# Kernel tuning notes

Hardware: AMD Instinct MI355X
Metric: run time of the kernel (lower is better)

Reference implementation:

```python
import jax, jax.numpy as jnp
import numpy as np

NUM_GRAPHS = 512
NODES_PER_GRAPH = 30
IN_CH = 8
HID = 64
NUM_LAYERS = 5
BRANCHES = 41
BN_EPS = 1e-5


def setup_inputs() -> dict:
    key = jax.random.key(0)
    ks = jax.random.split(key, 16)
    N = NUM_GRAPHS * NODES_PER_GRAPH
    x = jax.random.normal(ks[0], (N, IN_CH), jnp.float32)
    branch_u = jax.random.randint(ks[1], (BRANCHES,), 0, NODES_PER_GRAPH, jnp.int32)
    branch_v = jax.random.randint(ks[2], (BRANCHES,), 0, NODES_PER_GRAPH, jnp.int32)
    # Build bidirectional edge_index from the per-graph branch list + graph offsets
    offsets = (jnp.arange(NUM_GRAPHS, dtype=jnp.int32) * NODES_PER_GRAPH)
    u = (branch_u[None, :] + offsets[:, None]).reshape(-1)
    v = (branch_v[None, :] + offsets[:, None]).reshape(-1)
    edge_index = jnp.stack([jnp.concatenate([u, v]), jnp.concatenate([v, u])], axis=0)  # [2, E]
    s = 0.05
    inp = {
        'x': x, 'edge_index': edge_index, 'branch_u': branch_u, 'branch_v': branch_v,
        'num_graphs': NUM_GRAPHS,
        'Wp': jax.random.normal(ks[3], (IN_CH, HID), jnp.float32) * s,
        'bp': jnp.zeros((HID,), jnp.float32),
        'W1': jax.random.normal(ks[4], (NUM_LAYERS, 2 * HID, 32), jnp.float32) * s,
        'b1': jnp.zeros((NUM_LAYERS, 32), jnp.float32),
        'W2': jax.random.normal(ks[5], (NUM_LAYERS, 32, HID * HID), jnp.float32) * s,
        'b2': jnp.zeros((NUM_LAYERS, HID * HID), jnp.float32),
        'Wr': jax.random.normal(ks[6], (NUM_LAYERS, HID, HID), jnp.float32) * s,
        'br': jnp.zeros((NUM_LAYERS, HID), jnp.float32),
        'gamma': jnp.ones((NUM_LAYERS, HID), jnp.float32),
        'beta': jnp.zeros((NUM_LAYERS, HID), jnp.float32),
        'rmean': jax.random.normal(ks[7], (NUM_LAYERS, HID), jnp.float32) * s,
        'rvar': jax.random.uniform(ks[8], (NUM_LAYERS, HID), jnp.float32) + 0.5,
        'Wm1': jax.random.normal(ks[9], (2 * HID, HID), jnp.float32) * s,
        'bm1': jnp.zeros((HID,), jnp.float32),
        'Wm2': jax.random.normal(ks[10], (HID, 1), jnp.float32) * s,
        'bm2': jnp.zeros((1,), jnp.float32),
    }
    return inp


def reference(x, edge_index, branch_u, branch_v, num_graphs,
              Wp, bp, W1, b1, W2, b2, Wr, br,
              gamma, beta, rmean, rvar, Wm1, bm1, Wm2, bm2):
    N = x.shape[0]
    src, dst = edge_index[0], edge_index[1]  # messages flow src -> dst
    h = x @ Wp + bp  # [N, H]
    # in-degree for mean aggregation (clamped to avoid div-by-zero on isolated nodes)
    deg = jax.ops.segment_sum(jnp.ones(src.shape, h.dtype), dst, num_segments=N)
    deg = jnp.maximum(deg, 1.0)[:, None]
    for l in range(NUM_LAYERS):
        res = h
        ea = jnp.concatenate([h[src], h[dst]], axis=-1)              # [E, 2H] edge_attr
        w = jax.nn.relu(ea @ W1[l] + b1[l]) @ W2[l] + b2[l]          # [E, H*H]
        w = w.reshape(-1, HID, HID)                                  # [E, in, out]
        msg = jnp.einsum('eh,eho->eo', h[src], w)                    # gather + bmm
        agg = jax.ops.segment_sum(msg, dst, num_segments=N) / deg    # scatter-mean
        h2 = agg + h @ Wr[l] + br[l]                                 # NNConv root weight + bias
        # BatchNorm1d (eval mode: running stats)
        h2 = (h2 - rmean[l]) * (gamma[l] / jnp.sqrt(rvar[l] + BN_EPS)) + beta[l]
        h = jax.nn.relu(h2) + res                                    # dropout off (eval) + residual
    offsets = jnp.arange(num_graphs, dtype=src.dtype) * NODES_PER_GRAPH
    u_idx = (branch_u[None, :] + offsets[:, None]).reshape(-1)
    v_idx = (branch_v[None, :] + offsets[:, None]).reshape(-1)
    ef = jnp.concatenate([h[u_idx], h[v_idx]], axis=-1)              # [G*41, 2H]
    out = jax.nn.relu(ef @ Wm1 + bm1) @ Wm2 + bm2                    # [G*41, 1]
    return out
```

## Files before the change

kernel.cpp:

```cpp
#include <hip/hip_runtime.h>


typedef float f32x4 __attribute__((ext_vector_type(4)));
typedef _Float16 f16x8 __attribute__((ext_vector_type(8)));
typedef _Float16 f16x4 __attribute__((ext_vector_type(4)));

#define MFMA16(a, b, c) __builtin_amdgcn_mfma_f32_16x16x32_f16((a), (b), (c), 0, 0, 0)

#define WS_W2S 0u
#define WS_W1S 1351680u
#define WS_WRS 1392640u
#define WS_BNS 1433600u
#define WS_BNH 1434880u
#define WS_WM1H 1436160u
#define WS_WM1L 1452544u

__device__ inline f16x8 ld_frag_g(const _Float16* p) {
  union { uint4 u; f16x8 f; } c;
  c.u = *(const uint4*)p;
  return c.f;
}
__device__ inline f16x8 ld_frag_s(const _Float16* p) { return *(const f16x8*)p; }

__global__ __launch_bounds__(256) void prep_kernel(
    const float* __restrict__ W1, const float* __restrict__ W2,
    const float* __restrict__ b2, const float* __restrict__ Wr,
    const float* __restrict__ gamma, const float* __restrict__ beta,
    const float* __restrict__ rmean, const float* __restrict__ rvar,
    const float* __restrict__ Wm1, unsigned char* __restrict__ ws) {
  __shared__ __align__(16) float tile[32][68];
  const int tid = threadIdx.x;
  if (blockIdx.x < 330) {
    int l = blockIdx.x / 66, jb = blockIdx.x % 66;
    int s = tid >> 3, n0 = (tid & 7) * 8;
    int j = jb * 32 + s;
    const float* srcp = (j < 2048)
        ? (W2 + (size_t)l * 131072 + (size_t)j * 64 + n0)
        : (b2 + (size_t)l * 4096 + (size_t)(j - 2048) * 64 + n0);
    *(f32x4*)&tile[s][n0] = *(const f32x4*)srcp;
    *(f32x4*)&tile[s][n0 + 4] = *(const f32x4*)(srcp + 4);
    __syncthreads();
    int n = tid >> 2, sb = (tid & 3) * 8;
    f16x8 hv;
#pragma unroll
    for (int u = 0; u < 8; ++u) hv[u] = (_Float16)tile[sb + u][n];
    _Float16* dst = (_Float16*)(ws + WS_W2S) +
                    (size_t)l * 135168 + (size_t)jb * 2048 + n * 32 + sb;
    *(f16x8*)dst = hv;
    return;
  }
  int idx = (blockIdx.x - 330) * 256 + tid;
  _Float16* W1s = (_Float16*)(ws + WS_W1S);
  _Float16* Wrs = (_Float16*)(ws + WS_WRS);
  float* bns = (float*)(ws + WS_BNS);
  float* bnh = (float*)(ws + WS_BNH);
  _Float16* Wm1h = (_Float16*)(ws + WS_WM1H);
  _Float16* Wm1l = (_Float16*)(ws + WS_WM1L);
  if (idx < 20480) {
    int l = idx / 4096, r = idx % 4096;
    int t = r >> 10, n = (r >> 5) & 31, s2 = r & 31;
    int j = t * 32 + s2;
    W1s[idx] = (_Float16)W1[l * 4096 + j * 32 + n];
  } else if (idx < 40960) {
    int i3 = idx - 20480;
    int l = i3 / 4096, r = i3 % 4096;
    int t = r >> 11, rem = r & 2047;
    int n = rem >> 5, s2 = rem & 31;
    int j = t * 32 + s2;
    Wrs[i3] = (_Float16)Wr[l * 4096 + j * 64 + n];
  } else if (idx < 41280) {
    int i4 = idx - 40960;
    float sc = gamma[i4] * rsqrtf(rvar[i4] + 1e-5f);
    bns[i4] = sc;
    bnh[i4] = beta[i4] - rmean[i4] * sc;
  } else if (idx < 49472) {
    int i5 = idx - 41280;
    int t = i5 >> 11, n = (i5 >> 5) & 63, s2 = i5 & 31;
    float w = Wm1[(t * 32 + s2) * 64 + n];
    _Float16 hi = (_Float16)w;
    Wm1h[i5] = hi;
    Wm1l[i5] = (_Float16)(w - (float)hi);
  }
}

__global__ __launch_bounds__(512, 4) void gnn_kernel(
    const float* __restrict__ x, const int* __restrict__ bu, const int* __restrict__ bv,
    const float* __restrict__ Wp, const float* __restrict__ bp,
    const float* __restrict__ b1, const float* __restrict__ brr,
    const float* __restrict__ bm1, const float* __restrict__ Wm2,
    const float* __restrict__ bm2,
    const _Float16* __restrict__ W2s, const _Float16* __restrict__ W1s,
    const _Float16* __restrict__ Wrs, const _Float16* __restrict__ Wm1h,
    const _Float16* __restrict__ Wm1l,
    const float* __restrict__ bns, const float* __restrict__ bnh,
    float* __restrict__ out) {
  __shared__ __align__(16) float hF[32][68];
  __shared__ __align__(16) _Float16 hH[32][72];
  __shared__ __align__(16) _Float16 hL[32][72];
  __shared__ __align__(16) _Float16 zEh[96][40];
  __shared__ __align__(16) float agg[32][68];
  __shared__ __align__(16) float hid2[64][48];
  __shared__ int srcn[96], dstn[96];
  __shared__ float invdeg[32];

  const int tid = threadIdx.x;
  const int g = blockIdx.x;
  const int wv = tid >> 6;
  const int ln = tid & 63;
  const int q = ln >> 4;
  const int m16 = ln & 15;
  const f32x4 zero4 = {0.f, 0.f, 0.f, 0.f};

  if (tid < 96) {
    int s, d;
    if (tid < 41)      { s = bu[tid];      d = bv[tid]; }
    else if (tid < 82) { s = bv[tid - 41]; d = bu[tid - 41]; }
    else               { s = 0;            d = 0; }
    srcn[tid] = s; dstn[tid] = d;
  }
  if (tid < 136) { hF[30 + tid / 68][tid % 68] = 0.f; }
  if (tid < 144) {
    hH[30 + tid / 72][tid % 72] = (_Float16)0.f;
    hL[30 + tid / 72][tid % 72] = (_Float16)0.f;
  }
  for (int u = tid; u < 32 * 68; u += 512) ((float*)agg)[u] = 0.f;
  __syncthreads();
  if (tid < 32) {
    int cnt = 0;
    for (int e = 0; e < 82; ++e) cnt += (dstn[e] == tid) ? 1 : 0;
    invdeg[tid] = 1.0f / (float)(cnt > 0 ? cnt : 1);
  }
  for (int u = tid; u < 30 * 64; u += 512) {
    int n = u >> 6, c = u & 63;
    float acc = bp[c];
#pragma unroll
    for (int k = 0; k < 8; ++k) acc += x[(g * 30 + n) * 8 + k] * Wp[k * 64 + c];
    hF[n][c] = acc;
    _Float16 hi = (_Float16)acc;
    hH[n][c] = hi;
    hL[n][c] = (_Float16)(acc - (float)hi);
  }
  __syncthreads();

  for (int l = 0; l < 5; ++l) {
    const int ncolR = (wv & 3) * 16 + m16;
    const int mtR = wv >> 2;
    float scl = bns[l * 64 + ncolR];
    float sft = bnh[l * 64 + ncolR];
    float brb = brr[l * 64 + ncolR];
    f32x4 racc = zero4;
    {
      f16x8 wb0 = ld_frag_g(Wrs + ((l * 2 + 0) * 64 + ncolR) * 32 + q * 8);
      f16x8 wb1 = ld_frag_g(Wrs + ((l * 2 + 1) * 64 + ncolR) * 32 + q * 8);
      racc = MFMA16(ld_frag_s(&hH[mtR * 16 + m16][q * 8]), wb0, racc);
      racc = MFMA16(ld_frag_s(&hH[mtR * 16 + m16][32 + q * 8]), wb1, racc);
      racc = MFMA16(ld_frag_s(&hL[mtR * 16 + m16][q * 8]), wb0, racc);
      racc = MFMA16(ld_frag_s(&hL[mtR * 16 + m16][32 + q * 8]), wb1, racc);
    }
    {
      int ntz = wv & 1, g2 = wv >> 1;
      int ncol = ntz * 16 + m16;
      f16x8 bf[4];
#pragma unroll
      for (int t = 0; t < 4; ++t)
        bf[t] = ld_frag_g(W1s + ((l * 4 + t) * 32 + ncol) * 32 + q * 8);
      float b1v = b1[l * 32 + ncol];
#pragma unroll
      for (int mi = 0; mi < 2; ++mi) {
        int mt = g2 + mi * 4;
        if (mt < 6) {
          int e = mt * 16 + m16;
          int sn = srcn[e], dn = dstn[e];
          f32x4 acc = zero4;
#pragma unroll
          for (int t = 0; t < 4; ++t) {
            int nd = (t < 2) ? sn : dn;
            acc = MFMA16(ld_frag_s(&hH[nd][(t & 1) * 32 + q * 8]), bf[t], acc);
          }
#pragma unroll
          for (int t = 0; t < 4; ++t) {
            int nd = (t < 2) ? sn : dn;
            acc = MFMA16(ld_frag_s(&hL[nd][(t & 1) * 32 + q * 8]), bf[t], acc);
          }
#pragma unroll
          for (int r = 0; r < 4; ++r) {
            int e2 = mt * 16 + q * 4 + r;
            zEh[e2][ncol] = (_Float16)fmaxf(acc[r] + b1v, 0.f);
          }
        }
      }
    }
    __syncthreads();

    {
      int nt = wv & 3, mh = wv >> 2;
      int e0 = mh * 48 + m16, e1 = e0 + 16, e2 = e0 + 32;
      f16x8 hA[3][2];
      {
        int s0 = srcn[e0], s1 = srcn[e1], s2 = srcn[e2];
        hA[0][0] = ld_frag_s(&hH[s0][q * 8]); hA[0][1] = ld_frag_s(&hH[s0][32 + q * 8]);
        hA[1][0] = ld_frag_s(&hH[s1][q * 8]); hA[1][1] = ld_frag_s(&hH[s1][32 + q * 8]);
        hA[2][0] = ld_frag_s(&hH[s2][q * 8]); hA[2][1] = ld_frag_s(&hH[s2][32 + q * 8]);
      }
      f32x4 macc[3] = {zero4, zero4, zero4};
      const _Float16* Wb = W2s + (size_t)l * 135168 + (nt * 16 + m16) * 32 + q * 8;
      f16x8 r0a = ld_frag_g(Wb + (size_t)0 * 2048), r0b = ld_frag_g(Wb + (size_t)1 * 2048);
      f16x8 r1a = ld_frag_g(Wb + (size_t)2 * 2048), r1b = ld_frag_g(Wb + (size_t)3 * 2048);
      f16x8 r2a = ld_frag_g(Wb + (size_t)4 * 2048), r2b = ld_frag_g(Wb + (size_t)5 * 2048);
      f16x8 r3a, r3b;
      f16x8 Bz0 = ld_frag_g(Wb + (size_t)64 * 2048), Bz1 = ld_frag_g(Wb + (size_t)65 * 2048);
      macc[0] = MFMA16(hA[0][0], Bz0, macc[0]); macc[0] = MFMA16(hA[0][1], Bz1, macc[0]);
      macc[1] = MFMA16(hA[1][0], Bz0, macc[1]); macc[1] = MFMA16(hA[1][1], Bz1, macc[1]);
      macc[2] = MFMA16(hA[2][0], Bz0, macc[2]); macc[2] = MFMA16(hA[2][1], Bz1, macc[2]);
      f16x4 zc0 = *(const f16x4*)&zEh[e0][0];
      f16x4 zc1 = *(const f16x4*)&zEh[e1][0];
      f16x4 zc2 = *(const f16x4*)&zEh[e2][0];
      for (int cb = 0; cb < 32; cb += 4) {
        f16x4 zb0 = zc0, zb1 = zc1, zb2 = zc2;
        zc0 = *(const f16x4*)&zEh[e0][cb + 4];
        zc1 = *(const f16x4*)&zEh[e1][cb + 4];
        zc2 = *(const f16x4*)&zEh[e2][cb + 4];
        {
          r3a = ld_frag_g(Wb + (size_t)(2 * cb + 6) * 2048);
          r3b = ld_frag_g(Wb + (size_t)(2 * cb + 7) * 2048);
          _Float16 z0 = zb0[0], z1 = zb1[0], z2 = zb2[0];
          macc[0] = MFMA16(hA[0][0] * z0, r0a, macc[0]); macc[0] = MFMA16(hA[0][1] * z0, r0b, macc[0]);
          macc[1] = MFMA16(hA[1][0] * z1, r0a, macc[1]); macc[1] = MFMA16(hA[1][1] * z1, r0b, macc[1]);
          macc[2] = MFMA16(hA[2][0] * z2, r0a, macc[2]); macc[2] = MFMA16(hA[2][1] * z2, r0b, macc[2]);
        }
        {
          r0a = ld_frag_g(Wb + (size_t)(2 * cb + 8) * 2048);
          r0b = ld_frag_g(Wb + (size_t)(2 * cb + 9) * 2048);
          _Float16 z0 = zb0[1], z1 = zb1[1], z2 = zb2[1];
          macc[0] = MFMA16(hA[0][0] * z0, r1a, macc[0]); macc[0] = MFMA16(hA[0][1] * z0, r1b, macc[0]);
          macc[1] = MFMA16(hA[1][0] * z1, r1a, macc[1]); macc[1] = MFMA16(hA[1][1] * z1, r1b, macc[1]);
          macc[2] = MFMA16(hA[2][0] * z2, r1a, macc[2]); macc[2] = MFMA16(hA[2][1] * z2, r1b, macc[2]);
        }
        {
          r1a = ld_frag_g(Wb + (size_t)(2 * cb + 10) * 2048);
          r1b = ld_frag_g(Wb + (size_t)(2 * cb + 11) * 2048);
          _Float16 z0 = zb0[2], z1 = zb1[2], z2 = zb2[2];
          macc[0] = MFMA16(hA[0][0] * z0, r2a, macc[0]); macc[0] = MFMA16(hA[0][1] * z0, r2b, macc[0]);
          macc[1] = MFMA16(hA[1][0] * z1, r2a, macc[1]); macc[1] = MFMA16(hA[1][1] * z1, r2b, macc[1]);
          macc[2] = MFMA16(hA[2][0] * z2, r2a, macc[2]); macc[2] = MFMA16(hA[2][1] * z2, r2b, macc[2]);
        }
        {
          r2a = ld_frag_g(Wb + (size_t)(2 * cb + 12) * 2048);
          r2b = ld_frag_g(Wb + (size_t)(2 * cb + 13) * 2048);
          _Float16 z0 = zb0[3], z1 = zb1[3], z2 = zb2[3];
          macc[0] = MFMA16(hA[0][0] * z0, r3a, macc[0]); macc[0] = MFMA16(hA[0][1] * z0, r3b, macc[0]);
          macc[1] = MFMA16(hA[1][0] * z1, r3a, macc[1]); macc[1] = MFMA16(hA[1][1] * z1, r3b, macc[1]);
          macc[2] = MFMA16(hA[2][0] * z2, r3a, macc[2]); macc[2] = MFMA16(hA[2][1] * z2, r3b, macc[2]);
        }
      }
#pragma unroll
      for (int mi = 0; mi < 3; ++mi) {
#pragma unroll
        for (int r = 0; r < 4; ++r) {
          int e = mh * 48 + mi * 16 + q * 4 + r;
          if (e < 82) atomicAdd(&agg[dstn[e]][nt * 16 + m16], macc[mi][r]);
        }
      }
    }
    __syncthreads();

    {
#pragma unroll
      for (int r = 0; r < 4; ++r) {
        int row = mtR * 16 + q * 4 + r;
        if (row < 30) {
          float v = agg[row][ncolR] * invdeg[row] + racc[r] + brb;
          agg[row][ncolR] = 0.f;
          v = v * scl + sft;
          float hn = fmaxf(v, 0.f) + hF[row][ncolR];
          hF[row][ncolR] = hn;
          _Float16 hi = (_Float16)hn;
          hH[row][ncolR] = hi;
          hL[row][ncolR] = (_Float16)(hn - (float)hi);
        }
      }
    }
    __syncthreads();
  }

  {
    int nt = wv & 3, mtb = wv >> 2;
    int c = nt * 16 + m16;
    float bm1v = bm1[c];
    int nmt = (mtb == 0) ? 2 : 1;
    for (int p2 = 0; p2 < nmt; ++p2) {
      int mt = (p2 == 0) ? mtb : 2;
      int e = mt * 16 + m16;
      int un = srcn[e], vn = dstn[e];
      f32x4 acc = zero4;
#pragma unroll
      for (int t = 0; t < 4; ++t) {
        int nd = (t < 2) ? un : vn;
        int co = (t & 1) * 32 + q * 8;
        f16x8 bh2 = ld_frag_g(Wm1h + (t * 64 + c) * 32 + q * 8);
        f16x8 bl2 = ld_frag_g(Wm1l + (t * 64 + c) * 32 + q * 8);
        f16x8 ah = ld_frag_s(&hH[nd][co]);
        f16x8 al = ld_frag_s(&hL[nd][co]);
        acc = MFMA16(ah, bh2, acc);
        acc = MFMA16(al, bh2, acc);
        acc = MFMA16(ah, bl2, acc);
      }
      f32x4 res;
#pragma unroll
      for (int r = 0; r < 4; ++r) res[r] = fmaxf(acc[r] + bm1v, 0.f);
      *(f32x4*)&hid2[c][mt * 16 + (q << 2)] = res;
    }
  }
  __syncthreads();
  if (tid < 41) {
    float acc = bm2[0];
#pragma unroll 4
    for (int c = 0; c < 64; ++c) acc += hid2[c][tid] * Wm2[c];
    out[g * 41 + tid] = acc;
  }
}

extern "C" void kernel_launch(void* const* d_in, const int* in_sizes, int n_in,
                              void* d_out, int out_size, void* d_ws, size_t ws_size,
                              hipStream_t stream) {
  const float* x   = (const float*)d_in[0];
  const int* bu    = (const int*)d_in[2];
  const int* bv    = (const int*)d_in[3];
  const float* Wp  = (const float*)d_in[5];
  const float* bp  = (const float*)d_in[6];
  const float* W1  = (const float*)d_in[7];
  const float* b1  = (const float*)d_in[8];
  const float* W2  = (const float*)d_in[9];
  const float* b2  = (const float*)d_in[10];
  const float* Wr  = (const float*)d_in[11];
  const float* br  = (const float*)d_in[12];
  const float* gm  = (const float*)d_in[13];
  const float* bt  = (const float*)d_in[14];
  const float* rm  = (const float*)d_in[15];
  const float* rv  = (const float*)d_in[16];
  const float* Wm1 = (const float*)d_in[17];
  const float* bm1 = (const float*)d_in[18];
  const float* Wm2 = (const float*)d_in[19];
  const float* bm2 = (const float*)d_in[20];
  unsigned char* ws = (unsigned char*)d_ws;
  float* out = (float*)d_out;

  prep_kernel<<<524, 256, 0, stream>>>(W1, W2, b2, Wr, gm, bt, rm, rv, Wm1, ws);
  gnn_kernel<<<512, 512, 0, stream>>>(
      x, bu, bv, Wp, bp, b1, br, bm1, Wm2, bm2,
      (const _Float16*)(ws + WS_W2S),
      (const _Float16*)(ws + WS_W1S),
      (const _Float16*)(ws + WS_WRS),
      (const _Float16*)(ws + WS_WM1H),
      (const _Float16*)(ws + WS_WM1L),
      (const float*)(ws + WS_BNS),
      (const float*)(ws + WS_BNH),
      out);
}
```

Before: 220.0 us.

## Split root-weight MMA onto idle waves and seed aggregation buffer with it

Warp work is repartitioned so waves 0-5 compute the edge-network first layer while waves 6-7 compute the root-weight product h@Wr. They write that product, pre-multiplied by degree, straight into the agg buffer, so agg needs no separate zeroing and racc is no longer held in registers across the message phase. This is meant to balance MFMA work across waves and cut register pressure and zeroing stores. The cost is an extra multiply by degree followed by division, which adds a small rounding difference, and a narrower zEh padding that may change LDS bank conflicts.

```diff
diff --git a/kernel.cpp b/kernel.cpp
--- a/kernel.cpp
+++ b/kernel.cpp
@@ -97,11 +97,12 @@
   __shared__ __align__(16) float hF[32][68];
   __shared__ __align__(16) _Float16 hH[32][72];
   __shared__ __align__(16) _Float16 hL[32][72];
-  __shared__ __align__(16) _Float16 zEh[96][40];
+  __shared__ __align__(16) _Float16 zEh[96][36];
   __shared__ __align__(16) float agg[32][68];
   __shared__ __align__(16) float hid2[64][48];
   __shared__ int srcn[96], dstn[96];
   __shared__ float invdeg[32];
+  __shared__ float degf[32];
 
   const int tid = threadIdx.x;
   const int g = blockIdx.x;
@@ -123,12 +124,13 @@
     hH[30 + tid / 72][tid % 72] = (_Float16)0.f;
     hL[30 + tid / 72][tid % 72] = (_Float16)0.f;
   }
-  for (int u = tid; u < 32 * 68; u += 512) ((float*)agg)[u] = 0.f;
   __syncthreads();
   if (tid < 32) {
     int cnt = 0;
     for (int e = 0; e < 82; ++e) cnt += (dstn[e] == tid) ? 1 : 0;
-    invdeg[tid] = 1.0f / (float)(cnt > 0 ? cnt : 1);
+    int c1 = (cnt > 0) ? cnt : 1;
+    invdeg[tid] = 1.0f / (float)c1;
+    degf[tid] = (float)c1;
   }
   for (int u = tid; u < 30 * 64; u += 512) {
     int n = u >> 6, c = u & 63;
@@ -143,22 +145,9 @@
   __syncthreads();
 
   for (int l = 0; l < 5; ++l) {
-    const int ncolR = (wv & 3) * 16 + m16;
-    const int mtR = wv >> 2;
-    float scl = bns[l * 64 + ncolR];
-    float sft = bnh[l * 64 + ncolR];
-    float brb = brr[l * 64 + ncolR];
-    f32x4 racc = zero4;
-    {
-      f16x8 wb0 = ld_frag_g(Wrs + ((l * 2 + 0) * 64 + ncolR) * 32 + q * 8);
-      f16x8 wb1 = ld_frag_g(Wrs + ((l * 2 + 1) * 64 + ncolR) * 32 + q * 8);
-      racc = MFMA16(ld_frag_s(&hH[mtR * 16 + m16][q * 8]), wb0, racc);
-      racc = MFMA16(ld_frag_s(&hH[mtR * 16 + m16][32 + q * 8]), wb1, racc);
-      racc = MFMA16(ld_frag_s(&hL[mtR * 16 + m16][q * 8]), wb0, racc);
-      racc = MFMA16(ld_frag_s(&hL[mtR * 16 + m16][32 + q * 8]), wb1, racc);
-    }
-    {
-      int ntz = wv & 1, g2 = wv >> 1;
+    if (wv < 6) {
+      int ntz = (wv >= 3) ? 1 : 0;
+      int mtb = (wv % 3) * 2;
       int ncol = ntz * 16 + m16;
       f16x8 bf[4];
 #pragma unroll
@@ -167,25 +156,43 @@
       float b1v = b1[l * 32 + ncol];
 #pragma unroll
       for (int mi = 0; mi < 2; ++mi) {
-        int mt = g2 + mi * 4;
-        if (mt < 6) {
-          int e = mt * 16 + m16;
-          int sn = srcn[e], dn = dstn[e];
-          f32x4 acc = zero4;
-#pragma unroll
-          for (int t = 0; t < 4; ++t) {
-            int nd = (t < 2) ? sn : dn;
-            acc = MFMA16(ld_frag_s(&hH[nd][(t & 1) * 32 + q * 8]), bf[t], acc);
-          }
-#pragma unroll
-          for (int t = 0; t < 4; ++t) {
-            int nd = (t < 2) ? sn : dn;
-            acc = MFMA16(ld_frag_s(&hL[nd][(t & 1) * 32 + q * 8]), bf[t], acc);
-          }
+        int mt = mtb + mi;
+        int e = mt * 16 + m16;
+        int sn = srcn[e], dn = dstn[e];
+        f32x4 acc = zero4;
+#pragma unroll
+        for (int t = 0; t < 4; ++t) {
+          int nd = (t < 2) ? sn : dn;
+          acc = MFMA16(ld_frag_s(&hH[nd][(t & 1) * 32 + q * 8]), bf[t], acc);
+        }
+#pragma unroll
+        for (int t = 0; t < 4; ++t) {
+          int nd = (t < 2) ? sn : dn;
+          acc = MFMA16(ld_frag_s(&hL[nd][(t & 1) * 32 + q * 8]), bf[t], acc);
+        }
+#pragma unroll
+        for (int r = 0; r < 4; ++r) {
+          int e2 = mt * 16 + q * 4 + r;
+          zEh[e2][ncol] = (_Float16)fmaxf(acc[r] + b1v, 0.f);
+        }
+      }
+    } else {
+#pragma unroll
+      for (int nq = 0; nq < 2; ++nq) {
+        int ncolR = ((wv - 6) * 2 + nq) * 16 + m16;
+        f16x8 wb0 = ld_frag_g(Wrs + ((l * 2 + 0) * 64 + ncolR) * 32 + q * 8);
+        f16x8 wb1 = ld_frag_g(Wrs + ((l * 2 + 1) * 64 + ncolR) * 32 + q * 8);
+#pragma unroll
+        for (int mtR = 0; mtR < 2; ++mtR) {
+          f32x4 racc = zero4;
+          racc = MFMA16(ld_frag_s(&hH[mtR * 16 + m16][q * 8]), wb0, racc);
+          racc = MFMA16(ld_frag_s(&hH[mtR * 16 + m16][32 + q * 8]), wb1, racc);
+          racc = MFMA16(ld_frag_s(&hL[mtR * 16 + m16][q * 8]), wb0, racc);
+          racc = MFMA16(ld_frag_s(&hL[mtR * 16 + m16][32 + q * 8]), wb1, racc);
 #pragma unroll
           for (int r = 0; r < 4; ++r) {
-            int e2 = mt * 16 + q * 4 + r;
-            zEh[e2][ncol] = (_Float16)fmaxf(acc[r] + b1v, 0.f);
+            int row = mtR * 16 + q * 4 + r;
+            agg[row][ncolR] = racc[r] * degf[row & 31];
           }
         }
       }
@@ -265,18 +272,22 @@
     __syncthreads();
 
     {
+      const int ncolC = (wv & 3) * 16 + m16;
+      const int mtC = wv >> 2;
+      float scl = bns[l * 64 + ncolC];
+      float sft = bnh[l * 64 + ncolC];
+      float brb = brr[l * 64 + ncolC];
 #pragma unroll
       for (int r = 0; r < 4; ++r) {
-        int row = mtR * 16 + q * 4 + r;
+        int row = mtC * 16 + q * 4 + r;
         if (row < 30) {
-          float v = agg[row][ncolR] * invdeg[row] + racc[r] + brb;
-          agg[row][ncolR] = 0.f;
+          float v = agg[row][ncolC] * invdeg[row] + brb;
           v = v * scl + sft;
-          float hn = fmaxf(v, 0.f) + hF[row][ncolR];
-          hF[row][ncolR] = hn;
+          float hn = fmaxf(v, 0.f) + hF[row][ncolC];
+          hF[row][ncolC] = hn;
           _Float16 hi = (_Float16)hn;
-          hH[row][ncolR] = hi;
-          hL[row][ncolR] = (_Float16)(hn - (float)hi);
+          hH[row][ncolC] = hi;
+          hL[row][ncolC] = (_Float16)(hn - (float)hi);
         }
       }
     }
```

After: 219.7 us. About the same (-0.1%).
